# Optimization experiments

Hardware: AMD Instinct MI355X
Metric: run time of the kernel (lower is better)

The kernel has to match this reference:

```python
import jax, jax.numpy as jnp
import numpy as np

B, S, H = 8, 1024, 1024
NH, DH = 16, 64
F_DIM, E, TOPK = 4096, 8, 2
EPS = 1e-5


def setup_inputs() -> dict:
    key = jax.random.key(0)
    ks = jax.random.split(key, 12)
    s = 0.02
    return {
        "x": jax.random.normal(ks[0], (B, S, H), jnp.float32),
        "ln1_w": jnp.ones((H,), jnp.float32),
        "ln1_b": jnp.zeros((H,), jnp.float32),
        "ln2_w": jnp.ones((H,), jnp.float32),
        "ln2_b": jnp.zeros((H,), jnp.float32),
        "in_proj_w": jax.random.normal(ks[1], (3 * H, H), jnp.float32) * s,
        "in_proj_b": jnp.zeros((3 * H,), jnp.float32),
        "out_proj_w": jax.random.normal(ks[2], (H, H), jnp.float32) * s,
        "out_proj_b": jnp.zeros((H,), jnp.float32),
        "gate_w": jax.random.normal(ks[3], (E, H), jnp.float32) * s,
        "gate_b": jnp.zeros((E,), jnp.float32),
        "w1": jax.random.normal(ks[4], (E, H, F_DIM), jnp.float32) * s,
        "b1": jnp.zeros((E, F_DIM), jnp.float32),
        "w2": jax.random.normal(ks[5], (E, F_DIM, H), jnp.float32) * s,
        "b2": jnp.zeros((E, H), jnp.float32),
    }


def _layernorm(x, w, b):
    mu = jnp.mean(x, axis=-1, keepdims=True)
    var = jnp.var(x, axis=-1, keepdims=True)
    return (x - mu) * jax.lax.rsqrt(var + EPS) * w + b


def reference(x, ln1_w, ln1_b, ln2_w, ln2_b, in_proj_w, in_proj_b,
              out_proj_w, out_proj_b, gate_w, gate_b, w1, b1, w2, b2):
    # --- attention sub-block ---
    xn = _layernorm(x, ln1_w, ln1_b)
    qkv = xn @ in_proj_w.T + in_proj_b                     # [B,S,3H]
    q, k, v = jnp.split(qkv, 3, axis=-1)
    q = q.reshape(B, S, NH, DH).transpose(0, 2, 1, 3)      # [B,NH,S,DH]
    k = k.reshape(B, S, NH, DH).transpose(0, 2, 1, 3)
    v = v.reshape(B, S, NH, DH).transpose(0, 2, 1, 3)
    scores = jnp.einsum("bhqd,bhkd->bhqk", q, k) / jnp.sqrt(jnp.float32(DH))
    attn = jax.nn.softmax(scores, axis=-1)
    ctx = jnp.einsum("bhqk,bhkd->bhqd", attn, v)
    ctx = ctx.transpose(0, 2, 1, 3).reshape(B, S, H)
    x = x + ctx @ out_proj_w.T + out_proj_b

    # --- MoE sub-block (dense compute-all-experts, top-k combine) ---
    xn2 = _layernorm(x, ln2_w, ln2_b)
    logits = xn2 @ gate_w.T + gate_b                       # [B,S,E]
    topk_vals, topk_idx = jax.lax.top_k(logits, TOPK)      # [B,S,K]
    probs = jax.nn.softmax(topk_vals, axis=-1)
    hid = jax.nn.gelu(jnp.einsum("bsh,ehf->bsef", xn2, w1) + b1, approximate=False)
    expert_out = jnp.einsum("bsef,efh->bseh", hid, w2) + b2  # [B,S,E,H]
    selected = jnp.take_along_axis(expert_out, topk_idx[..., None], axis=2)  # [B,S,K,H]
    moe_out = jnp.sum(probs[..., None] * selected, axis=2)
    return x + moe_out
```

## Files before the change

kernel.cpp:

```cpp
#include <hip/hip_runtime.h>
#include <math.h>

typedef unsigned short u16;
typedef short short8 __attribute__((ext_vector_type(8)));
typedef float f32x4 __attribute__((ext_vector_type(4)));
typedef unsigned short us4 __attribute__((ext_vector_type(4)));

#define NTOK 8192
#define NEXP 8

__device__ __forceinline__ u16 f2bf(float f) {
  union { float f; unsigned u; } v; v.f = f;
  unsigned r = v.u + 0x7FFFu + ((v.u >> 16) & 1u);
  return (u16)(r >> 16);
}
__device__ __forceinline__ float bf2f(u16 u) {
  union { unsigned u; float f; } v; v.u = ((unsigned)u) << 16; return v.f;
}
__device__ __forceinline__ void gload16(const u16* src, u16* ldsDst) {
  __builtin_amdgcn_global_load_lds(
    (const __attribute__((address_space(1))) unsigned int*)(const void*)src,
    (__attribute__((address_space(3))) unsigned int*)(void*)ldsDst, 16, 0, 0);
}

__global__ void cast_kernel(const float* __restrict__ in, u16* __restrict__ out, int n4) {
  int i = blockIdx.x * blockDim.x + threadIdx.x;
  if (i < n4) {
    float4 v = ((const float4*)in)[i];
    us4 o;
    o[0] = f2bf(v.x); o[1] = f2bf(v.y); o[2] = f2bf(v.z); o[3] = f2bf(v.w);
    ((us4*)out)[i] = o;
  }
}

__global__ void transpose_cast(const float* __restrict__ in, u16* __restrict__ out, int R, int C) {
  __shared__ float tile[64][65];
  const size_t eoff = (size_t)blockIdx.z * (size_t)R * (size_t)C;
  in += eoff; out += eoff;
  const int rb = blockIdx.y * 64, cb = blockIdx.x * 64;
  const int tid = threadIdx.x;
  const int lr4 = tid >> 4;
  const int lc4 = (tid & 15) * 4;
#pragma unroll
  for (int p = 0; p < 4; ++p) {
    float4 v = *(const float4*)&in[(size_t)(rb + p * 16 + lr4) * C + cb + lc4];
    tile[p * 16 + lr4][lc4 + 0] = v.x;
    tile[p * 16 + lr4][lc4 + 1] = v.y;
    tile[p * 16 + lr4][lc4 + 2] = v.z;
    tile[p * 16 + lr4][lc4 + 3] = v.w;
  }
  __syncthreads();
  const int oc = tid >> 3;
  const int orr = (tid & 7) * 8;
#pragma unroll
  for (int p = 0; p < 2; ++p) {
    int c = p * 32 + oc;
    short8 o;
#pragma unroll
    for (int j = 0; j < 8; ++j) o[j] = (short)f2bf(tile[orr + j][c]);
    *(short8*)&out[(size_t)(cb + c) * R + rb + orr] = o;
  }
}

__global__ void ln1_kernel(const float* __restrict__ x, const float* __restrict__ w,
                           const float* __restrict__ b, u16* __restrict__ xn) {
  const int t = blockIdx.x, tid = threadIdx.x;
  __shared__ float red[8];
  float4 v = ((const float4*)(x + (size_t)t * 1024))[tid];
  float s  = v.x + v.y + v.z + v.w;
  float sq = v.x*v.x + v.y*v.y + v.z*v.z + v.w*v.w;
#pragma unroll
  for (int m = 1; m < 64; m <<= 1) { s += __shfl_xor(s, m, 64); sq += __shfl_xor(sq, m, 64); }
  if ((tid & 63) == 0) { red[tid >> 6] = s; red[4 + (tid >> 6)] = sq; }
  __syncthreads();
  float S = red[0] + red[1] + red[2] + red[3];
  float Q = red[4] + red[5] + red[6] + red[7];
  float mu  = S * (1.0f / 1024.0f);
  float var = Q * (1.0f / 1024.0f) - mu * mu;
  float inv = rsqrtf(var + 1e-5f);
  float4 wv = ((const float4*)w)[tid];
  float4 bv = ((const float4*)b)[tid];
  us4 o;
  o[0] = f2bf((v.x - mu) * inv * wv.x + bv.x);
  o[1] = f2bf((v.y - mu) * inv * wv.y + bv.y);
  o[2] = f2bf((v.z - mu) * inv * wv.z + bv.z);
  o[3] = f2bf((v.w - mu) * inv * wv.w + bv.w);
  ((us4*)(xn + (size_t)t * 1024))[tid] = o;
}

__global__ void ln2_gate_kernel(const float* __restrict__ x2, const float* __restrict__ w,
                                const float* __restrict__ b, const float* __restrict__ gw,
                                const float* __restrict__ gb, u16* __restrict__ xn2,
                                int* __restrict__ cnt, int* __restrict__ list_tok,
                                float* __restrict__ list_prob, int* __restrict__ tok2slot) {
  const int t = blockIdx.x, tid = threadIdx.x;
  __shared__ float red[8];
  __shared__ float logits[NEXP];
  __shared__ float xrow[1024];
  float4 v = ((const float4*)(x2 + (size_t)t * 1024))[tid];
  float s  = v.x + v.y + v.z + v.w;
  float sq = v.x*v.x + v.y*v.y + v.z*v.z + v.w*v.w;
#pragma unroll
  for (int m = 1; m < 64; m <<= 1) { s += __shfl_xor(s, m, 64); sq += __shfl_xor(sq, m, 64); }
  if ((tid & 63) == 0) { red[tid >> 6] = s; red[4 + (tid >> 6)] = sq; }
  __syncthreads();
  float S = red[0] + red[1] + red[2] + red[3];
  float Q = red[4] + red[5] + red[6] + red[7];
  float mu  = S * (1.0f / 1024.0f);
  float var = Q * (1.0f / 1024.0f) - mu * mu;
  float inv = rsqrtf(var + 1e-5f);
  float4 wv = ((const float4*)w)[tid];
  float4 bv = ((const float4*)b)[tid];
  float n0 = (v.x - mu) * inv * wv.x + bv.x;
  float n1 = (v.y - mu) * inv * wv.y + bv.y;
  float n2 = (v.z - mu) * inv * wv.z + bv.z;
  float n3 = (v.w - mu) * inv * wv.w + bv.w;
  xrow[tid*4+0] = n0; xrow[tid*4+1] = n1; xrow[tid*4+2] = n2; xrow[tid*4+3] = n3;
  us4 o; o[0] = f2bf(n0); o[1] = f2bf(n1); o[2] = f2bf(n2); o[3] = f2bf(n3);
  ((us4*)(xn2 + (size_t)t * 1024))[tid] = o;
  __syncthreads();
  int e = tid >> 5, l32 = tid & 31;
  const float* gwe = gw + e * 1024;
  float part = 0.0f;
  for (int i = l32; i < 1024; i += 32) part += xrow[i] * gwe[i];
#pragma unroll
  for (int m = 1; m < 32; m <<= 1) part += __shfl_xor(part, m, 64);
  if (l32 == 0) logits[e] = part + gb[e];
  __syncthreads();
  if (tid == 0) {
    float v0 = -1e30f; int e0 = 0;
#pragma unroll
    for (int i = 0; i < NEXP; ++i) { float L = logits[i]; if (L > v0) { v0 = L; e0 = i; } }
    float v1 = -1e30f; int e1 = 0;
#pragma unroll
    for (int i = 0; i < NEXP; ++i) { if (i == e0) continue; float L = logits[i]; if (L > v1) { v1 = L; e1 = i; } }
    float texp = expf(v1 - v0);
    float p0 = 1.0f / (1.0f + texp);
    float p1 = texp / (1.0f + texp);
    int s0 = atomicAdd(&cnt[e0], 1);
    list_tok[e0 * NTOK + s0] = t; list_prob[e0 * NTOK + s0] = p0;
    int s1 = atomicAdd(&cnt[e1], 1);
    list_tok[e1 * NTOK + s1] = t; list_prob[e1 * NTOK + s1] = p1;
    if (tok2slot) {
      tok2slot[2 * t]     = e0 * NTOK + s0;
      tok2slot[2 * t + 1] = e1 * NTOK + s1;
    }
  }
}

__launch_bounds__(256)
__global__ void attn_kernel(const u16* __restrict__ qkv, u16* __restrict__ ctx) {
  const int bh = blockIdx.y;
  const int b = bh >> 4, h = bh & 15;
  const int q0 = blockIdx.x * 64;
  const int tokBase = b * 1024;
  __shared__ __align__(16) u16 Qs[64 * 72];
  __shared__ __align__(16) u16 Ks[64 * 72];
  __shared__ __align__(16) u16 Vts[64 * 72];
  __shared__ __align__(16) u16 Ps[64 * 72];
  const int tid = threadIdx.x;
  const int wave = tid >> 6, lane = tid & 63, g = lane >> 4, lr = lane & 15;

  {
    int r = tid >> 2, d0 = (tid & 3) * 16;
    const u16* src = qkv + (size_t)(tokBase + q0 + r) * 3072 + h * 64 + d0;
    *(short8*)&Qs[r * 72 + d0]     = *(const short8*)src;
    *(short8*)&Qs[r * 72 + d0 + 8] = *(const short8*)(src + 8);
  }
  __syncthreads();
  short8 aq0 = *(const short8*)&Qs[(wave * 16 + lr) * 72 + g * 8];
  short8 aq1 = *(const short8*)&Qs[(wave * 16 + lr) * 72 + 32 + g * 8];

  const f32x4 zf = {0.f, 0.f, 0.f, 0.f};
  f32x4 Ofr[4] = {zf, zf, zf, zf};
  float m_run[4], l_run[4];
#pragma unroll
  for (int r = 0; r < 4; ++r) { m_run[r] = -1e30f; l_run[r] = 0.f; }

  for (int kt = 0; kt < 1024; kt += 64) {
    __syncthreads();
    {
      int r = tid >> 2, d0 = (tid & 3) * 16;
      const u16* ksrc = qkv + (size_t)(tokBase + kt + r) * 3072 + 1024 + h * 64 + d0;
      *(short8*)&Ks[r * 72 + d0]     = *(const short8*)ksrc;
      *(short8*)&Ks[r * 72 + d0 + 8] = *(const short8*)(ksrc + 8);
      const u16* vsrc = qkv + (size_t)(tokBase + kt + r) * 3072 + 2048 + h * 64 + d0;
      short8 v0 = *(const short8*)vsrc, v1 = *(const short8*)(vsrc + 8);
#pragma unroll
      for (int j = 0; j < 8; ++j) Vts[(d0 + j) * 72 + r] = (u16)v0[j];
#pragma unroll
      for (int j = 0; j < 8; ++j) Vts[(d0 + 8 + j) * 72 + r] = (u16)v1[j];
    }
    __syncthreads();
    f32x4 sf[4];
#pragma unroll
    for (int n = 0; n < 4; ++n) sf[n] = zf;
#pragma unroll
    for (int n = 0; n < 4; ++n) {
      short8 bk0 = *(const short8*)&Ks[(n * 16 + lr) * 72 + g * 8];
      short8 bk1 = *(const short8*)&Ks[(n * 16 + lr) * 72 + 32 + g * 8];
      sf[n] = __builtin_amdgcn_mfma_f32_16x16x32_bf16(aq0, bk0, sf[n], 0, 0, 0);
      sf[n] = __builtin_amdgcn_mfma_f32_16x16x32_bf16(aq1, bk1, sf[n], 0, 0, 0);
    }
#pragma unroll
    for (int n = 0; n < 4; ++n)
#pragma unroll
      for (int r = 0; r < 4; ++r) sf[n][r] *= 0.125f;
    float mnew[4], sc[4];
#pragma unroll
    for (int r = 0; r < 4; ++r) {
      float t0 = fmaxf(fmaxf(sf[0][r], sf[1][r]), fmaxf(sf[2][r], sf[3][r]));
#pragma unroll
      for (int msk = 1; msk < 16; msk <<= 1) t0 = fmaxf(t0, __shfl_xor(t0, msk, 64));
      mnew[r] = fmaxf(m_run[r], t0);
      sc[r] = __expf(m_run[r] - mnew[r]);
      m_run[r] = mnew[r];
    }
#pragma unroll
    for (int n = 0; n < 4; ++n)
#pragma unroll
      for (int r = 0; r < 4; ++r) sf[n][r] = __expf(sf[n][r] - mnew[r]);
#pragma unroll
    for (int r = 0; r < 4; ++r) {
      float s0 = sf[0][r] + sf[1][r] + sf[2][r] + sf[3][r];
#pragma unroll
      for (int msk = 1; msk < 16; msk <<= 1) s0 += __shfl_xor(s0, msk, 64);
      l_run[r] = l_run[r] * sc[r] + s0;
    }
#pragma unroll
    for (int nd = 0; nd < 4; ++nd)
#pragma unroll
      for (int r = 0; r < 4; ++r) Ofr[nd][r] *= sc[r];
#pragma unroll
    for (int n = 0; n < 4; ++n)
#pragma unroll
      for (int r = 0; r < 4; ++r)
        Ps[(wave * 16 + g * 4 + r) * 72 + n * 16 + lr] = f2bf(sf[n][r]);
    __syncthreads();
    short8 ap0 = *(const short8*)&Ps[(wave * 16 + lr) * 72 + g * 8];
    short8 ap1 = *(const short8*)&Ps[(wave * 16 + lr) * 72 + 32 + g * 8];
#pragma unroll
    for (int nd = 0; nd < 4; ++nd) {
      short8 bv0 = *(const short8*)&Vts[(nd * 16 + lr) * 72 + g * 8];
      short8 bv1 = *(const short8*)&Vts[(nd * 16 + lr) * 72 + 32 + g * 8];
      Ofr[nd] = __builtin_amdgcn_mfma_f32_16x16x32_bf16(ap0, bv0, Ofr[nd], 0, 0, 0);
      Ofr[nd] = __builtin_amdgcn_mfma_f32_16x16x32_bf16(ap1, bv1, Ofr[nd], 0, 0, 0);
    }
  }
#pragma unroll
  for (int nd = 0; nd < 4; ++nd)
#pragma unroll
    for (int r = 0; r < 4; ++r) {
      int tok = tokBase + q0 + wave * 16 + g * 4 + r;
      int col = h * 64 + nd * 16 + lr;
      ctx[(size_t)tok * 1024 + col] = f2bf(Ofr[nd][r] / l_run[r]);
    }
}

template<int EPI>
__launch_bounds__(512, 2)
__global__ void gemm256(const u16* __restrict__ Abase, const u16* __restrict__ Bbase,
                        int K, int lda, int N, int ldc,
                        const float* __restrict__ bias,
                        const float* __restrict__ resid,
                        float* __restrict__ outF,
                        u16* __restrict__ outB,
                        const int* __restrict__ cnt,
                        const int* __restrict__ list_tok,
                        const float* __restrict__ list_prob) {
  const int gx = gridDim.x, gy = gridDim.y;
  int nwg = gx * gy * gridDim.z;
  int orig = blockIdx.x + blockIdx.y * gx + blockIdx.z * gx * gy;
  int q8 = nwg >> 3, r8 = nwg & 7, xcd = orig & 7, lid = orig >> 3;
  int wg = (xcd < r8 ? xcd * (q8 + 1) : r8 * (q8 + 1) + (xcd - r8) * q8) + lid;
  const int bz = wg / (gx * gy); int rem = wg - bz * gx * gy;
  const int n0 = (rem % gx) * 256;
  const int m0 = (rem / gx) * 256;
  const int e  = bz;

  int M = NTOK;
  int slotBase = 0;
  const u16* Bw = Bbase;
  const float* biasp = bias;
  if constexpr (EPI >= 2) {
    for (int j = 0; j < e; ++j) slotBase += cnt[j];
    M = cnt[e];
    if (m0 >= M) return;
    Bw += (size_t)e * (size_t)N * (size_t)K;
    biasp = bias + (size_t)e * N;
  }

  __shared__ __align__(16) u16 As[2 * 16384];
  __shared__ __align__(16) u16 Bs[2 * 16384];

  const int tid = threadIdx.x;
  const int wave = tid >> 6, lane = tid & 63, g = lane >> 4, lr = lane & 15;
  const int wm = wave >> 2, wn = wave & 3;

  size_t aoff[4], boff[4];
#pragma unroll
  for (int i = 0; i < 4; ++i) {
    int ci = i * 512 + tid;
    int row = ci >> 3, c = ci & 7;
    int lc = c ^ (row & 7);
    int arow;
    if constexpr (EPI == 2) {
      int ridx = m0 + row; if (ridx > M - 1) ridx = M - 1;
      arow = list_tok[e * NTOK + ridx];
    } else if constexpr (EPI >= 3) {
      int ridx = m0 + row; if (ridx > M - 1) ridx = M - 1;
      arow = slotBase + ridx;
    } else {
      arow = m0 + row;
    }
    aoff[i] = (size_t)arow * (size_t)lda + (size_t)(lc << 3);
    boff[i] = (size_t)(n0 + row) * (size_t)K + (size_t)(lc << 3);
  }

  const int NT = K >> 6;

#define STAGE(T) do { int _t = (T); if (_t < NT) { int _b = (_t & 1) << 14; int _kt = _t << 6; \
    _Pragma("unroll") for (int i = 0; i < 4; ++i) \
      gload16(Abase + aoff[i] + _kt, &As[_b + ((i * 512 + wave * 64) << 3)]); \
    _Pragma("unroll") for (int i = 0; i < 4; ++i) \
      gload16(Bw + boff[i] + _kt, &Bs[_b + ((i * 512 + wave * 64) << 3)]); } } while (0)

  const int sw = lr & 7;
  const int abase = (wm * 128 + lr) * 64;
  const int bbase = (wn * 64 + lr) * 64;
  const int sk0 = (g ^ sw) * 8;
  const int sk1 = ((4 + g) ^ sw) * 8;

  const f32x4 zf = {0.f, 0.f, 0.f, 0.f};
  f32x4 acc[8][4];
#pragma unroll
  for (int m = 0; m < 8; ++m)
#pragma unroll
    for (int n = 0; n < 4; ++n) acc[m][n] = zf;

  STAGE(0);
  STAGE(1);

  for (int t = 0; t < NT; ++t) {
    if (t < NT - 1) { asm volatile("s_waitcnt vmcnt(8)" ::: "memory"); }
    else           { asm volatile("s_waitcnt vmcnt(0)" ::: "memory"); }
    __builtin_amdgcn_s_barrier();
    asm volatile("" ::: "memory");
    const u16* Ab = As + ((t & 1) << 14);
    const u16* Bb = Bs + ((t & 1) << 14);
    short8 bfr[2][4];
#pragma unroll
    for (int n = 0; n < 4; ++n) bfr[0][n] = *(const short8*)&Bb[bbase + n * 1024 + sk0];
#pragma unroll
    for (int n = 0; n < 4; ++n) bfr[1][n] = *(const short8*)&Bb[bbase + n * 1024 + sk1];
    short8 afr[8];
#pragma unroll
    for (int m = 0; m < 8; ++m) afr[m] = *(const short8*)&Ab[abase + m * 1024 + sk0];
    __builtin_amdgcn_s_setprio(1);
#pragma unroll
    for (int m = 0; m < 8; ++m)
#pragma unroll
      for (int n = 0; n < 4; ++n)
        acc[m][n] = __builtin_amdgcn_mfma_f32_16x16x32_bf16(afr[m], bfr[0][n], acc[m][n], 0, 0, 0);
    __builtin_amdgcn_s_setprio(0);
#pragma unroll
    for (int m = 0; m < 8; ++m) afr[m] = *(const short8*)&Ab[abase + m * 1024 + sk1];
    asm volatile("s_waitcnt lgkmcnt(0)" ::: "memory");
    __builtin_amdgcn_s_barrier();
    asm volatile("" ::: "memory");
    STAGE(t + 2);
    __builtin_amdgcn_s_setprio(1);
#pragma unroll
    for (int m = 0; m < 8; ++m)
#pragma unroll
      for (int n = 0; n < 4; ++n)
        acc[m][n] = __builtin_amdgcn_mfma_f32_16x16x32_bf16(afr[m], bfr[1][n], acc[m][n], 0, 0, 0);
    __builtin_amdgcn_s_setprio(0);
  }
#undef STAGE

#pragma unroll
  for (int m = 0; m < 8; ++m) {
    int rloc = wm * 128 + m * 16 + g * 4;
#pragma unroll
    for (int n = 0; n < 4; ++n) {
      int gc = n0 + wn * 64 + n * 16 + lr;
      float bcol = biasp[gc];
#pragma unroll
      for (int r = 0; r < 4; ++r) {
        int ridx = m0 + rloc + r;
        float vv = acc[m][n][r] + bcol;
        if constexpr (EPI == 0) {
          outB[(size_t)ridx * ldc + gc] = f2bf(vv);
        } else if constexpr (EPI == 1) {
          size_t off = (size_t)ridx * ldc + gc;
          outF[off] = vv + resid[off];
        } else if constexpr (EPI == 2) {
          if (ridx < M)
            outB[(size_t)(slotBase + ridx) * ldc + gc] =
              f2bf(0.5f * vv * (1.0f + erff(vv * 0.70710678f)));
        } else if constexpr (EPI == 3) {
          if (ridx < M)
            outB[(size_t)(slotBase + ridx) * ldc + gc] = f2bf(vv);
        } else {
          if (ridx < M) {
            int tok = list_tok[e * NTOK + ridx];
            float p = list_prob[e * NTOK + ridx];
            atomicAdd(&outF[(size_t)tok * ldc + gc], vv * p);
          }
        }
      }
    }
  }
}

__global__ void combine_kernel(const u16* __restrict__ part, const int* __restrict__ cnt,
                               const int* __restrict__ tok2slot, const float* __restrict__ lprb,
                               float* __restrict__ out) {
  const int t = blockIdx.x, tid = threadIdx.x;
  __shared__ int base[NEXP];
  if (tid == 0) {
    int b = 0;
#pragma unroll
    for (int j = 0; j < NEXP; ++j) { base[j] = b; b += cnt[j]; }
  }
  __syncthreads();
  int c0 = tok2slot[2 * t], c1 = tok2slot[2 * t + 1];
  float p0 = lprb[c0], p1 = lprb[c1];
  int g0 = base[c0 >> 13] + (c0 & 8191);
  int g1 = base[c1 >> 13] + (c1 & 8191);
  us4 a = ((const us4*)(part + (size_t)g0 * 1024))[tid];
  us4 b = ((const us4*)(part + (size_t)g1 * 1024))[tid];
  float4 o = ((const float4*)(out + (size_t)t * 1024))[tid];
  o.x += p0 * bf2f(a[0]) + p1 * bf2f(b[0]);
  o.y += p0 * bf2f(a[1]) + p1 * bf2f(b[1]);
  o.z += p0 * bf2f(a[2]) + p1 * bf2f(b[2]);
  o.w += p0 * bf2f(a[3]) + p1 * bf2f(b[3]);
  ((float4*)(out + (size_t)t * 1024))[tid] = o;
}

extern "C" void kernel_launch(void* const* d_in, const int* in_sizes, int n_in,
                              void* d_out, int out_size, void* d_ws, size_t ws_size,
                              hipStream_t stream) {
  const float* x    = (const float*)d_in[0];
  const float* ln1w = (const float*)d_in[1];
  const float* ln1b = (const float*)d_in[2];
  const float* ln2w = (const float*)d_in[3];
  const float* ln2b = (const float*)d_in[4];
  const float* inw  = (const float*)d_in[5];
  const float* inb  = (const float*)d_in[6];
  const float* outw = (const float*)d_in[7];
  const float* outb = (const float*)d_in[8];
  const float* gw   = (const float*)d_in[9];
  const float* gb   = (const float*)d_in[10];
  const float* w1   = (const float*)d_in[11];
  const float* b1   = (const float*)d_in[12];
  const float* w2   = (const float*)d_in[13];
  const float* b2   = (const float*)d_in[14];
  float* out = (float*)d_out;
  char* ws = (char*)d_ws;

  u16* xn1 = (u16*)(ws + 0);
  u16* qkv = (u16*)(ws + 16777216);
  u16* ctx = (u16*)(ws + 67108864);
  u16* hid = (u16*)(ws + 0);
  u16* xn2 = (u16*)(ws + 134217728);
  u16* w1t = (u16*)(ws + 150994944);
  u16* winb  = (u16*)(ws + 218103808);
  u16* woutb = (u16*)(ws + 224395264);
  u16* w2t = (u16*)(ws + 134217728);
  u16* part = (u16*)(ws + 201326592);

  const bool bigWS = ws_size >= 235471872ull;
  int*   cnt, *ltok, *t2s; float* lprb;
  if (bigWS) {
    cnt  = (int*)(ws + 234881024);
    ltok = (int*)(ws + 234882048);
    lprb = (float*)(ws + 235144192);
    t2s  = (int*)(ws + 235406336);
  } else {
    cnt  = (int*)(ws + 226492416);
    ltok = (int*)(ws + 226492672);
    lprb = (float*)(ws + 226754816);
    t2s  = nullptr;
  }

  cast_kernel<<<3072, 256, 0, stream>>>(inw, winb, 786432);
  cast_kernel<<<1024, 256, 0, stream>>>(outw, woutb, 262144);
  transpose_cast<<<dim3(64, 16, 8), 256, 0, stream>>>(w1, w1t, 1024, 4096);

  ln1_kernel<<<8192, 256, 0, stream>>>(x, ln1w, ln1b, xn1);
  gemm256<0><<<dim3(12, 32, 1), 512, 0, stream>>>(xn1, winb, 1024, 1024, 3072, 3072,
                                                  inb, nullptr, nullptr, qkv, nullptr, nullptr, nullptr);
  attn_kernel<<<dim3(16, 128), 256, 0, stream>>>(qkv, ctx);
  gemm256<1><<<dim3(4, 32, 1), 512, 0, stream>>>(ctx, woutb, 1024, 1024, 1024, 1024,
                                                 outb, x, out, nullptr, nullptr, nullptr, nullptr);

  hipMemsetAsync(cnt, 0, 32, stream);
  ln2_gate_kernel<<<8192, 256, 0, stream>>>(out, ln2w, ln2b, gw, gb, xn2, cnt, ltok, lprb, t2s);
  gemm256<2><<<dim3(16, 32, 8), 512, 0, stream>>>(xn2, w1t, 1024, 1024, 4096, 4096,
                                                  b1, nullptr, nullptr, hid, cnt, ltok, lprb);
  transpose_cast<<<dim3(16, 64, 8), 256, 0, stream>>>(w2, w2t, 4096, 1024);
  if (bigWS) {
    gemm256<3><<<dim3(4, 32, 8), 512, 0, stream>>>(hid, w2t, 4096, 4096, 1024, 1024,
                                                   b2, nullptr, nullptr, part, cnt, ltok, lprb);
    combine_kernel<<<8192, 256, 0, stream>>>(part, cnt, t2s, lprb, out);
  } else {
    gemm256<4><<<dim3(4, 32, 8), 512, 0, stream>>>(hid, w2t, 4096, 4096, 1024, 1024,
                                                   b2, nullptr, out, nullptr, cnt, ltok, lprb);
  }
}
```

Before: 1.082 ms.

## Split GEMM main loop into four quadrant phases interleaving LDS reads and global prefetch

Restructures the gemm256 k-loop so each 64-wide k tile is processed in four MFMA phases, one per 4x2 quadrant of the accumulator. LDS fragment reads and global-to-LDS prefetch of the next-next tile are split into pieces that are issued between those phases, using s_barrier and sched_barrier to control ordering. The aim is to overlap memory traffic with MFMA work at finer grain than the previous two-phase loop. Launch bounds drop to one block per CU, giving more registers per wave at the cost of less occupancy to hide latency. The extra barriers add synchronisation overhead.

```diff
diff --git a/kernel.cpp b/kernel.cpp
--- a/kernel.cpp
+++ b/kernel.cpp
@@ -258,7 +258,7 @@
 }
 
 template<int EPI>
-__launch_bounds__(512, 2)
+__launch_bounds__(512, 1)
 __global__ void gemm256(const u16* __restrict__ Abase, const u16* __restrict__ Bbase,
                         int K, int lda, int N, int ldc,
                         const float* __restrict__ bias,
@@ -319,9 +319,13 @@
 
   const int NT = K >> 6;
 
-#define STAGE(T) do { int _t = (T); if (_t < NT) { int _b = (_t & 1) << 14; int _kt = _t << 6; \
-    _Pragma("unroll") for (int i = 0; i < 4; ++i) \
-      gload16(Abase + aoff[i] + _kt, &As[_b + ((i * 512 + wave * 64) << 3)]); \
+#define S_ALO(T) do { int _t = (T); if (_t < NT) { int _b = (_t & 1) << 14; int _kt = _t << 6; \
+    gload16(Abase + aoff[0] + _kt, &As[_b + ((0 * 512 + wave * 64) << 3)]); \
+    gload16(Abase + aoff[2] + _kt, &As[_b + ((2 * 512 + wave * 64) << 3)]); } } while (0)
+#define S_AHI(T) do { int _t = (T); if (_t < NT) { int _b = (_t & 1) << 14; int _kt = _t << 6; \
+    gload16(Abase + aoff[1] + _kt, &As[_b + ((1 * 512 + wave * 64) << 3)]); \
+    gload16(Abase + aoff[3] + _kt, &As[_b + ((3 * 512 + wave * 64) << 3)]); } } while (0)
+#define S_B(T) do { int _t = (T); if (_t < NT) { int _b = (_t & 1) << 14; int _kt = _t << 6; \
     _Pragma("unroll") for (int i = 0; i < 4; ++i) \
       gload16(Bw + boff[i] + _kt, &Bs[_b + ((i * 512 + wave * 64) << 3)]); } } while (0)
 
@@ -338,46 +342,95 @@
 #pragma unroll
     for (int n = 0; n < 4; ++n) acc[m][n] = zf;
 
-  STAGE(0);
-  STAGE(1);
+  S_ALO(0); S_B(0); S_AHI(0);
+  S_ALO(1); S_B(1); S_AHI(1);
+  if (NT >= 2) { asm volatile("s_waitcnt vmcnt(8)" ::: "memory"); }
+  else         { asm volatile("s_waitcnt vmcnt(0)" ::: "memory"); }
+  __builtin_amdgcn_s_barrier();
 
   for (int t = 0; t < NT; ++t) {
-    if (t < NT - 1) { asm volatile("s_waitcnt vmcnt(8)" ::: "memory"); }
-    else           { asm volatile("s_waitcnt vmcnt(0)" ::: "memory"); }
-    __builtin_amdgcn_s_barrier();
-    asm volatile("" ::: "memory");
     const u16* Ab = As + ((t & 1) << 14);
     const u16* Bb = Bs + ((t & 1) << 14);
-    short8 bfr[2][4];
-#pragma unroll
-    for (int n = 0; n < 4; ++n) bfr[0][n] = *(const short8*)&Bb[bbase + n * 1024 + sk0];
-#pragma unroll
-    for (int n = 0; n < 4; ++n) bfr[1][n] = *(const short8*)&Bb[bbase + n * 1024 + sk1];
-    short8 afr[8];
-#pragma unroll
-    for (int m = 0; m < 8; ++m) afr[m] = *(const short8*)&Ab[abase + m * 1024 + sk0];
+    short8 afr[4][2], bfr[4][2];
+#pragma unroll
+    for (int m = 0; m < 4; ++m) {
+      afr[m][0] = *(const short8*)&Ab[abase + m * 1024 + sk0];
+      afr[m][1] = *(const short8*)&Ab[abase + m * 1024 + sk1];
+    }
+#pragma unroll
+    for (int n = 0; n < 2; ++n) {
+      bfr[n][0] = *(const short8*)&Bb[bbase + n * 1024 + sk0];
+      bfr[n][1] = *(const short8*)&Bb[bbase + n * 1024 + sk1];
+    }
+    __builtin_amdgcn_s_barrier();
+    asm volatile("s_waitcnt lgkmcnt(0)" ::: "memory");
+    __builtin_amdgcn_sched_barrier(0);
     __builtin_amdgcn_s_setprio(1);
 #pragma unroll
-    for (int m = 0; m < 8; ++m)
-#pragma unroll
-      for (int n = 0; n < 4; ++n)
-        acc[m][n] = __builtin_amdgcn_mfma_f32_16x16x32_bf16(afr[m], bfr[0][n], acc[m][n], 0, 0, 0);
+    for (int kk = 0; kk < 2; ++kk)
+#pragma unroll
+      for (int m = 0; m < 4; ++m)
+#pragma unroll
+        for (int n = 0; n < 2; ++n)
+          acc[m][n] = __builtin_amdgcn_mfma_f32_16x16x32_bf16(afr[m][kk], bfr[n][kk], acc[m][n], 0, 0, 0);
     __builtin_amdgcn_s_setprio(0);
-#pragma unroll
-    for (int m = 0; m < 8; ++m) afr[m] = *(const short8*)&Ab[abase + m * 1024 + sk1];
+    __builtin_amdgcn_s_barrier();
+#pragma unroll
+    for (int n = 2; n < 4; ++n) {
+      bfr[n][0] = *(const short8*)&Bb[bbase + n * 1024 + sk0];
+      bfr[n][1] = *(const short8*)&Bb[bbase + n * 1024 + sk1];
+    }
+    S_ALO(t + 2);
+    __builtin_amdgcn_s_barrier();
     asm volatile("s_waitcnt lgkmcnt(0)" ::: "memory");
-    __builtin_amdgcn_s_barrier();
-    asm volatile("" ::: "memory");
-    STAGE(t + 2);
+    __builtin_amdgcn_sched_barrier(0);
     __builtin_amdgcn_s_setprio(1);
 #pragma unroll
-    for (int m = 0; m < 8; ++m)
-#pragma unroll
-      for (int n = 0; n < 4; ++n)
-        acc[m][n] = __builtin_amdgcn_mfma_f32_16x16x32_bf16(afr[m], bfr[1][n], acc[m][n], 0, 0, 0);
+    for (int kk = 0; kk < 2; ++kk)
+#pragma unroll
+      for (int m = 0; m < 4; ++m)
+#pragma unroll
+        for (int n = 2; n < 4; ++n)
+          acc[m][n] = __builtin_amdgcn_mfma_f32_16x16x32_bf16(afr[m][kk], bfr[n][kk], acc[m][n], 0, 0, 0);
     __builtin_amdgcn_s_setprio(0);
-  }
-#undef STAGE
+    __builtin_amdgcn_s_barrier();
+#pragma unroll
+    for (int m = 0; m < 4; ++m) {
+      afr[m][0] = *(const short8*)&Ab[abase + (m + 4) * 1024 + sk0];
+      afr[m][1] = *(const short8*)&Ab[abase + (m + 4) * 1024 + sk1];
+    }
+    S_B(t + 2);
+    __builtin_amdgcn_s_barrier();
+    asm volatile("s_waitcnt lgkmcnt(0)" ::: "memory");
+    __builtin_amdgcn_sched_barrier(0);
+    __builtin_amdgcn_s_setprio(1);
+#pragma unroll
+    for (int kk = 0; kk < 2; ++kk)
+#pragma unroll
+      for (int m = 0; m < 4; ++m)
+#pragma unroll
+        for (int n = 0; n < 2; ++n)
+          acc[m + 4][n] = __builtin_amdgcn_mfma_f32_16x16x32_bf16(afr[m][kk], bfr[n][kk], acc[m + 4][n], 0, 0, 0);
+    __builtin_amdgcn_s_setprio(0);
+    __builtin_amdgcn_s_barrier();
+    S_AHI(t + 2);
+    if (t < NT - 2) { asm volatile("s_waitcnt vmcnt(8)" ::: "memory"); }
+    else            { asm volatile("s_waitcnt vmcnt(0)" ::: "memory"); }
+    __builtin_amdgcn_s_barrier();
+    __builtin_amdgcn_s_setprio(1);
+#pragma unroll
+    for (int kk = 0; kk < 2; ++kk)
+#pragma unroll
+      for (int m = 0; m < 4; ++m)
+#pragma unroll
+        for (int n = 2; n < 4; ++n)
+          acc[m + 4][n] = __builtin_amdgcn_mfma_f32_16x16x32_bf16(afr[m][kk], bfr[n][kk], acc[m + 4][n], 0, 0, 0);
+    __builtin_amdgcn_s_setprio(0);
+    __builtin_amdgcn_s_barrier();
+  }
+#undef S_ALO
+#undef S_AHI
+#undef S_B
 
 #pragma unroll
   for (int m = 0; m < 8; ++m) {
```

Measured after the change: 1.147 ms. 1.06x slower.
